# Kernel optimization log

Hardware: AMD Instinct MI355X
Metric: run time of the kernel (lower is better)

Reference implementation:

```python
import jax, jax.numpy as jnp
from jax import lax
import numpy as np

T, B, I, H = 512, 64, 512, 512


def setup_inputs() -> dict:
    key = jax.random.key(0)
    k0, k1, k2, k3, k4 = jax.random.split(key, 5)
    s = 1.0 / np.sqrt(H)  # PyTorch LSTM init range
    x = jax.random.normal(k0, (T, B, I), dtype=jnp.float32)
    W_ih = jax.random.uniform(k1, (4 * H, I), jnp.float32, -s, s)
    W_hh = jax.random.uniform(k2, (4 * H, H), jnp.float32, -s, s)
    b_ih = jax.random.uniform(k3, (4 * H,), jnp.float32, -s, s)
    b_hh = jax.random.uniform(k4, (4 * H,), jnp.float32, -s, s)
    return {"x": x, "W_ih": W_ih, "W_hh": W_hh, "b_ih": b_ih, "b_hh": b_hh}


def reference(x, W_ih, W_hh, b_ih, b_hh):
    # x: [T, B, I] (seq-first, like nn.LSTM with batch_first=False)
    Bv = x.shape[1]
    Hv = W_hh.shape[1]
    # Precompute input projections for all timesteps: [T, B, 4H]
    x_proj = jnp.einsum('tbi,gi->tbg', x, W_ih) + b_ih + b_hh

    def step(carry, xp):
        h, c = carry
        gates = xp + h @ W_hh.T  # [B, 4H]
        i, f, g, o = jnp.split(gates, 4, axis=-1)  # PyTorch gate order i,f,g,o
        i = jax.nn.sigmoid(i)
        f = jax.nn.sigmoid(f)
        g = jnp.tanh(g)
        o = jax.nn.sigmoid(o)
        c = f * c + i * g
        h = o * jnp.tanh(c)
        return (h, c), h

    h0 = jnp.zeros((Bv, Hv), dtype=x.dtype)
    c0 = jnp.zeros((Bv, Hv), dtype=x.dtype)
    _, ys = lax.scan(step, (h0, c0), x_proj)
    return ys  # [T, B, H]
```

## Files before the change

### kernel.cpp

```cpp
#include <hip/hip_runtime.h>


#define T_STEPS 512
#define BATCH   64
#define HID     512
#define NB      64

typedef short bf16x8 __attribute__((ext_vector_type(8)));
typedef float f32x4  __attribute__((ext_vector_type(4)));

struct U16B { unsigned long long x, y; };

__device__ __forceinline__ unsigned short f2bf(float f) {
    unsigned int u = __builtin_bit_cast(unsigned int, f);
    u += 0x7FFFu + ((u >> 16) & 1u);
    return (unsigned short)(u >> 16);
}
__device__ __forceinline__ unsigned int pack2(float lo, float hi) {
    return (unsigned int)f2bf(lo) | ((unsigned int)f2bf(hi) << 16);
}
__device__ __forceinline__ uint4 cvt8(const float* __restrict__ p) {
    float4 f0 = *(const float4*)p;
    float4 f1 = *(const float4*)(p + 4);
    uint4 r;
    r.x = pack2(f0.x, f0.y);
    r.y = pack2(f0.z, f0.w);
    r.z = pack2(f1.x, f1.y);
    r.w = pack2(f1.z, f1.w);
    return r;
}
__device__ __forceinline__ bf16x8 load_h16(const void* p) {
    const unsigned long long* q = (const unsigned long long*)p;
    U16B v;
    v.x = __hip_atomic_load(q,     __ATOMIC_RELAXED, __HIP_MEMORY_SCOPE_AGENT);
    v.y = __hip_atomic_load(q + 1, __ATOMIC_RELAXED, __HIP_MEMORY_SCOPE_AGENT);
    return __builtin_bit_cast(bf16x8, v);
}
__device__ __forceinline__ void store_cg16(void* p, uint4 v) {
    unsigned long long* q = (unsigned long long*)p;
    U16B u = __builtin_bit_cast(U16B, v);
    __hip_atomic_store(q,     u.x, __ATOMIC_RELAXED, __HIP_MEMORY_SCOPE_AGENT);
    __hip_atomic_store(q + 1, u.y, __ATOMIC_RELAXED, __HIP_MEMORY_SCOPE_AGENT);
}
__device__ __forceinline__ float sigmoidf_(float x) {
    return 1.0f / (1.0f + __expf(-x));
}
__device__ __forceinline__ float tanhf_(float x) {
    x = fminf(fmaxf(x, -15.f), 15.f);
    float e = __expf(2.0f * x);
    return (e - 1.0f) / (e + 1.0f);
}

extern "C" __global__ void __launch_bounds__(256, 1)
lstm_fused(const float* __restrict__ x,
           const float* __restrict__ W_ih,
           const float* __restrict__ W_hh,
           const float* __restrict__ b_ih,
           const float* __restrict__ b_hh,
           float* __restrict__ out,
           unsigned int* __restrict__ flags,
           unsigned short* __restrict__ hbuf)
{
    __shared__ uint4 sB[2][2][16][64];
    __shared__ __align__(16) unsigned short sH[4][16][8];

    const int blk  = blockIdx.x;
    const int tid  = threadIdx.x;
    const int w    = tid >> 6;
    const int lane = tid & 63;
    const int l15  = lane & 15;
    const int quad = lane >> 4;
    const int hc0  = blk * 8;

    for (int u = tid; u < 2 * 16 * 64; u += 256) {
        int nt   = u >> 10;
        int kk   = (u >> 6) & 15;
        int ln   = u & 63;
        int c    = (ln & 15) + (nt << 4);
        int grow = ((c >> 3) << 9) + hc0 + (c & 7);
        int k0   = kk * 32 + ((ln >> 4) << 3);
        sB[0][nt][kk][ln] = cvt8(W_ih + grow * 512 + k0);
        sB[1][nt][kk][ln] = cvt8(W_hh + grow * 512 + k0);
    }

    float bias0, bias1;
    {
        int c0 = l15,      g0 = ((c0 >> 3) << 9) + hc0 + (c0 & 7);
        int c1 = l15 + 16, g1 = ((c1 >> 3) << 9) + hc0 + (c1 & 7);
        bias0 = b_ih[g0] + b_hh[g0];
        bias1 = b_ih[g1] + b_hh[g1];
    }
    __syncthreads();

    float cst[4] = {0.f, 0.f, 0.f, 0.f};
    const int aoff = (((w << 4) + l15) * 512) + (quad << 3);
    char* const hb_base = (char*)hbuf;
    const int   hread_off = (quad << 10) + (((w << 4) + l15) << 4);
    long long budget = 50000000LL;

    for (int t = 0; t < T_STEPS; ++t) {
        f32x4 acc0 = {0.f, 0.f, 0.f, 0.f};
        f32x4 acc1 = {0.f, 0.f, 0.f, 0.f};

        const float* xt = x + (size_t)t * (BATCH * 512) + aoff;
#pragma unroll
        for (int kk = 0; kk < 16; ++kk) {
            bf16x8 a  = __builtin_bit_cast(bf16x8, cvt8(xt + kk * 32));
            bf16x8 b0 = __builtin_bit_cast(bf16x8, sB[0][0][kk][lane]);
            bf16x8 b1 = __builtin_bit_cast(bf16x8, sB[0][1][kk][lane]);
            acc0 = __builtin_amdgcn_mfma_f32_16x16x32_bf16(a, b0, acc0, 0, 0, 0);
            acc1 = __builtin_amdgcn_mfma_f32_16x16x32_bf16(a, b1, acc1, 0, 0, 0);
        }

        if (t > 0) {
            if (w == 0) {
                const unsigned int* fp = flags + (size_t)(t - 1) * NB + lane;
                while (budget > 0) {
                    unsigned int v = __hip_atomic_load(fp, __ATOMIC_RELAXED,
                                                       __HIP_MEMORY_SCOPE_AGENT);
                    if (__all(v != 0)) break;
                    --budget;
                }
            }
            __syncthreads();

            const char* hp = hb_base + (((t - 1) & 1) << 16) + hread_off;
#pragma unroll
            for (int kk = 0; kk < 16; ++kk) {
                bf16x8 a  = load_h16(hp + (kk << 12));
                bf16x8 b0 = __builtin_bit_cast(bf16x8, sB[1][0][kk][lane]);
                bf16x8 b1 = __builtin_bit_cast(bf16x8, sB[1][1][kk][lane]);
                acc0 = __builtin_amdgcn_mfma_f32_16x16x32_bf16(a, b0, acc0, 0, 0, 0);
                acc1 = __builtin_amdgcn_mfma_f32_16x16x32_bf16(a, b1, acc1, 0, 0, 0);
            }
        }

        float gi[4], gf[4], gg[4], go[4];
#pragma unroll
        for (int r = 0; r < 4; ++r) {
            float a0 = acc0[r] + bias0;
            float a1 = acc1[r] + bias1;
            float p0 = __shfl_xor(a0, 8, 64);
            float p1 = __shfl_xor(a1, 8, 64);
            gi[r] = a0; gg[r] = a1; gf[r] = p0; go[r] = p1;
        }
        float hv[4];
        if (l15 < 8) {
#pragma unroll
            for (int r = 0; r < 4; ++r) {
                float iv = sigmoidf_(gi[r]);
                float fv = sigmoidf_(gf[r]);
                float gv = tanhf_(gg[r]);
                float ov = sigmoidf_(go[r]);
                cst[r] = fv * cst[r] + iv * gv;
                hv[r] = ov * tanhf_(cst[r]);
                sH[w][(quad << 2) + r][l15] = f2bf(hv[r]);
            }
        }
        asm volatile("s_waitcnt lgkmcnt(0)" ::: "memory");
        if (lane < 16) {
            uint4 v = *(const uint4*)&sH[w][lane][0];
            char* dst = hb_base + ((t & 1) << 16) + (blk << 10)
                        + (((w << 4) + lane) << 4);
            store_cg16(dst, v);
        }
        asm volatile("s_waitcnt vmcnt(0)" ::: "memory");
        __syncthreads();
        if (tid == 0) {
            __hip_atomic_store(flags + (size_t)t * NB + blk, 1u,
                               __ATOMIC_RELAXED, __HIP_MEMORY_SCOPE_AGENT);
        }

        if (l15 < 8) {
            const int rbase = (w << 4) + (quad << 2);
            float* op = out + (size_t)t * (BATCH * HID) + hc0 + l15;
#pragma unroll
            for (int r = 0; r < 4; ++r)
                op[(size_t)(rbase + r) * HID] = hv[r];
        }
    }
}

extern "C" void kernel_launch(void* const* d_in, const int* in_sizes, int n_in,
                              void* d_out, int out_size, void* d_ws, size_t ws_size,
                              hipStream_t stream) {
    const float* x    = (const float*)d_in[0];
    const float* W_ih = (const float*)d_in[1];
    const float* W_hh = (const float*)d_in[2];
    const float* b_ih = (const float*)d_in[3];
    const float* b_hh = (const float*)d_in[4];
    float* out = (float*)d_out;

    unsigned int*   flags = (unsigned int*)d_ws;
    const size_t    flag_bytes = (size_t)T_STEPS * NB * sizeof(unsigned int);
    unsigned short* hbuf  = (unsigned short*)((char*)d_ws + flag_bytes);

    (void)hipMemsetAsync(flags, 0, flag_bytes, stream);

    hipLaunchKernelGGL(lstm_fused, dim3(NB), dim3(256), 0, stream,
                       x, W_ih, W_hh, b_ih, b_hh, out, flags, hbuf);
}
```

Before: 4.321 ms.

## Replace per-block flag array with atomic counter barrier and vectorize output stores

Each timestep's grid barrier changes from 64 per-block flags polled by a full wavefront to one atomic counter per step, padded to 16 entries. Thread 0 alone polls it with s_sleep backoff. The fp32 hidden output is staged in shared memory so it can be written with 16-byte vector stores instead of scattered scalar stores. The contended atomic and the sleep may add latency to the critical path, and the spin budget drops sharply, which risks proceeding before all blocks have arrived if waits are long.

```diff
diff --git a/kernel.cpp b/kernel.cpp
--- a/kernel.cpp
+++ b/kernel.cpp
@@ -5,6 +5,7 @@
 #define BATCH   64
 #define HID     512
 #define NB      64
+#define CNT_STRIDE 16
 
 typedef short bf16x8 __attribute__((ext_vector_type(8)));
 typedef float f32x4  __attribute__((ext_vector_type(4)));
@@ -58,11 +59,12 @@
            const float* __restrict__ b_ih,
            const float* __restrict__ b_hh,
            float* __restrict__ out,
-           unsigned int* __restrict__ flags,
+           unsigned int* __restrict__ cnt,
            unsigned short* __restrict__ hbuf)
 {
     __shared__ uint4 sB[2][2][16][64];
     __shared__ __align__(16) unsigned short sH[4][16][8];
+    __shared__ __align__(16) float          sHf[4][16][8];
 
     const int blk  = blockIdx.x;
     const int tid  = threadIdx.x;
@@ -96,7 +98,7 @@
     const int aoff = (((w << 4) + l15) * 512) + (quad << 3);
     char* const hb_base = (char*)hbuf;
     const int   hread_off = (quad << 10) + (((w << 4) + l15) << 4);
-    long long budget = 50000000LL;
+    long long budget = 300000LL;
 
     for (int t = 0; t < T_STEPS; ++t) {
         f32x4 acc0 = {0.f, 0.f, 0.f, 0.f};
@@ -113,12 +115,13 @@
         }
 
         if (t > 0) {
-            if (w == 0) {
-                const unsigned int* fp = flags + (size_t)(t - 1) * NB + lane;
+            if (tid == 0) {
+                const unsigned int* cp = cnt + (size_t)(t - 1) * CNT_STRIDE;
                 while (budget > 0) {
-                    unsigned int v = __hip_atomic_load(fp, __ATOMIC_RELAXED,
+                    unsigned int v = __hip_atomic_load(cp, __ATOMIC_RELAXED,
                                                        __HIP_MEMORY_SCOPE_AGENT);
-                    if (__all(v != 0)) break;
+                    if (v >= NB) break;
+                    __builtin_amdgcn_s_sleep(1);
                     --budget;
                 }
             }
@@ -144,7 +147,6 @@
             float p1 = __shfl_xor(a1, 8, 64);
             gi[r] = a0; gg[r] = a1; gf[r] = p0; go[r] = p1;
         }
-        float hv[4];
         if (l15 < 8) {
 #pragma unroll
             for (int r = 0; r < 4; ++r) {
@@ -153,8 +155,9 @@
                 float gv = tanhf_(gg[r]);
                 float ov = sigmoidf_(go[r]);
                 cst[r] = fv * cst[r] + iv * gv;
-                hv[r] = ov * tanhf_(cst[r]);
-                sH[w][(quad << 2) + r][l15] = f2bf(hv[r]);
+                float hv = ov * tanhf_(cst[r]);
+                sH [w][(quad << 2) + r][l15] = f2bf(hv);
+                sHf[w][(quad << 2) + r][l15] = hv;
             }
         }
         asm volatile("s_waitcnt lgkmcnt(0)" ::: "memory");
@@ -167,16 +170,17 @@
         asm volatile("s_waitcnt vmcnt(0)" ::: "memory");
         __syncthreads();
         if (tid == 0) {
-            __hip_atomic_store(flags + (size_t)t * NB + blk, 1u,
-                               __ATOMIC_RELAXED, __HIP_MEMORY_SCOPE_AGENT);
-        }
-
-        if (l15 < 8) {
-            const int rbase = (w << 4) + (quad << 2);
-            float* op = out + (size_t)t * (BATCH * HID) + hc0 + l15;
-#pragma unroll
-            for (int r = 0; r < 4; ++r)
-                op[(size_t)(rbase + r) * HID] = hv[r];
+            (void)__hip_atomic_fetch_add(cnt + (size_t)t * CNT_STRIDE, 1u,
+                                         __ATOMIC_RELAXED, __HIP_MEMORY_SCOPE_AGENT);
+        }
+
+        if (lane < 32) {
+            int row  = lane & 15;
+            int half = lane >> 4;
+            uint4 v = *(const uint4*)&sHf[w][row][half << 2];
+            float* op = out + (size_t)t * (BATCH * HID)
+                        + (size_t)((w << 4) + row) * HID + hc0 + (half << 2);
+            *(uint4*)op = v;
         }
     }
 }
@@ -191,12 +195,12 @@
     const float* b_hh = (const float*)d_in[4];
     float* out = (float*)d_out;
 
-    unsigned int*   flags = (unsigned int*)d_ws;
-    const size_t    flag_bytes = (size_t)T_STEPS * NB * sizeof(unsigned int);
-    unsigned short* hbuf  = (unsigned short*)((char*)d_ws + flag_bytes);
-
-    (void)hipMemsetAsync(flags, 0, flag_bytes, stream);
+    unsigned int*   cnt = (unsigned int*)d_ws;
+    const size_t    cnt_bytes = (size_t)T_STEPS * CNT_STRIDE * sizeof(unsigned int);
+    unsigned short* hbuf = (unsigned short*)((char*)d_ws + cnt_bytes);
+
+    (void)hipMemsetAsync(cnt, 0, cnt_bytes, stream);
 
     hipLaunchKernelGGL(lstm_fused, dim3(NB), dim3(256), 0, stream,
-                       x, W_ih, W_hh, b_ih, b_hh, out, flags, hbuf);
-}
+                       x, W_ih, W_hh, b_ih, b_hh, out, cnt, hbuf);
+}
```

Result: no change. 4.298 ms (-0.5%).
